# Kernel tuning notes

Measured on AMD Instinct MI355X. Metric: run time of the kernel, lower is better.

## Reference

```python
import jax, jax.numpy as jnp
import numpy as np
import math

HEIGHT = 256
THRESH = int(HEIGHT / (2 * math.sqrt(2)))  # 90, as in Spectral_Discriminator.__init__
EPS = 1e-8


def _radial_bins(h, w):
    # Static (numpy) integer radius of each pixel from the spectrum center.
    y, x = np.indices((h, w))
    cx, cy = (w - 1) / 2.0, (h - 1) / 2.0
    r = np.hypot(x - cx, y - cy)
    r_int = r.astype(np.int64).ravel()           # [h*w]
    nbins = int(r_int.max()) + 1                 # ~ h/sqrt(2) + 1 bins
    return jnp.asarray(r_int), nbins


def get_fft_feature(x):
    # x: [B, 3, H, W] -> azimuthally averaged log power spectrum [B, nbins]
    gray = 0.2989 * x[:, 0] + 0.5870 * x[:, 1] + 0.1140 * x[:, 2]   # [B,H,W]
    f = jnp.fft.fft2(gray)                                           # complex64
    mag = jnp.log(jnp.abs(f) + EPS)                                  # log magnitude
    mag = jnp.fft.fftshift(mag, axes=(-2, -1))                       # center DC
    B, h, w = mag.shape
    r_int, nbins = _radial_bins(h, w)
    flat = mag.reshape(B, -1)                                        # [B, h*w]
    # radial (azimuthal-average) binning: segment mean by integer radius
    sums = jax.vmap(lambda v: jax.ops.segment_sum(v, r_int, num_segments=nbins))(flat)
    counts = jax.ops.segment_sum(jnp.ones((h * w,), jnp.float32), r_int, num_segments=nbins)
    prof = sums / counts                                             # [B, nbins]
    # per-sample min-max normalization (NaN if max==min; masked by caller)
    mn = prof.min(axis=1, keepdims=True)
    mx = prof.max(axis=1, keepdims=True)
    return (prof - mn) / (mx - mn)


def setup_inputs() -> dict:
    key = jax.random.key(0)
    k1, k2 = jax.random.split(key)
    x = jax.random.normal(k1, (128, 3, HEIGHT, HEIGHT), dtype=jnp.float32)
    w = jax.random.normal(k2, (1, THRESH), dtype=jnp.float32) * (1.0 / math.sqrt(THRESH))
    b = jnp.zeros((1,), dtype=jnp.float32)
    return {"x": x, "w": w, "b": b}


def reference(x, w, b):
    feat = get_fft_feature(x)                          # [B, nbins]
    feat = jnp.where(jnp.isnan(feat), 0.0, feat)       # nan-masking as in forward
    feat = feat[:, -THRESH:]                           # high-frequency tail
    return feat @ w.T + b                              # [B, 1]
```

## Files before the change

kernel.cpp:

```cpp
#include <hip/hip_runtime.h>
#include <hip/hip_fp16.h>
#include <math.h>

#define NB 128
#define N 256
#define NBINS 181
#define THRESH 90
#define RS 136
#define GS 264
#define BST 137

__device__ __forceinline__ int br4(int i) {
    return ((i&1)<<3) | ((i&2)<<1) | ((i&4)>>1) | ((i&8)>>3);
}

__device__ const float TW16R[8] = { 1.f,  0.92387953f,  0.70710678f,  0.38268343f,
                                    0.f, -0.38268343f, -0.70710678f, -0.92387953f };
__device__ const float TW16I[8] = { 0.f, -0.38268343f, -0.70710678f, -0.92387953f,
                                   -1.f, -0.92387953f, -0.70710678f, -0.38268343f };
__device__ const float W256R[16] = {
    1.00000000f, 0.99969882f, 0.99879546f, 0.99729046f, 0.99518473f, 0.99247953f,
    0.98917651f, 0.98527764f, 0.98078528f, 0.97570213f, 0.97003125f, 0.96377607f,
    0.95694034f, 0.94952818f, 0.94154407f, 0.93299280f };
__device__ const float W256I[16] = {
    -0.00000000f, -0.02454123f, -0.04906767f, -0.07356456f, -0.09801714f, -0.12241068f,
    -0.14673047f, -0.17096189f, -0.19509032f, -0.21910124f, -0.24298018f, -0.26671276f,
    -0.29028468f, -0.31368174f, -0.33688985f, -0.35989504f };

__device__ __forceinline__ void fft16(float2 v[16]) {
    #pragma unroll
    for (int s = 0; s < 4; ++s) {
        const int half = 1 << s;
        #pragma unroll
        for (int gg = 0; gg < 16; gg += 2*half) {
            #pragma unroll
            for (int j = 0; j < half; ++j) {
                const float wr = TW16R[j << (3 - s)];
                const float wi = TW16I[j << (3 - s)];
                float2 a = v[gg + j], b = v[gg + j + half];
                float tr = b.x*wr - b.y*wi;
                float ti = b.x*wi + b.y*wr;
                v[gg + j]        = make_float2(a.x + tr, a.y + ti);
                v[gg + j + half] = make_float2(a.x - tr, a.y - ti);
            }
        }
    }
}

__device__ __forceinline__ void twiddle256(float2 v[16], int l) {
    const float c = W256R[l], s = W256I[l];
    float wr = c, wi = s;
    #pragma unroll
    for (int k = 1; k < 16; ++k) {
        float xr = v[k].x, xi = v[k].y;
        v[k] = make_float2(xr*wr - xi*wi, xr*wi + xi*wr);
        float nr = wr*c - wi*s;
        float ni = wr*s + wi*c;
        wr = nr; wi = ni;
    }
}

__global__ __launch_bounds__(128) void row_fft_kernel(const float* __restrict__ x,
                                                      __half2* __restrict__ F) {
    __shared__ float2 zbuf[8*GS];

    const int t = threadIdx.x;
    const int b = blockIdx.y;
    const int pbase = blockIdx.x * 8;

    const int cidx = t & 63;
    const int sub  = t >> 6;
    const float* xb = x + (size_t)b * 3 * N * N;
    #pragma unroll
    for (int i = 0; i < 4; ++i) {
        int p  = i*2 + sub;
        int r0 = (pbase + p) * 2;
        const float* p0 = xb + (size_t)r0 * N + cidx*4;
        float4 a0 = *(const float4*)(p0);
        float4 a1 = *(const float4*)(p0 + N*N);
        float4 a2 = *(const float4*)(p0 + 2*N*N);
        float4 b0 = *(const float4*)(p0 + N);
        float4 b1 = *(const float4*)(p0 + N*N + N);
        float4 b2 = *(const float4*)(p0 + 2*N*N + N);
        float gx[4], gy[4];
        #pragma unroll
        for (int j = 0; j < 4; ++j) {
            gx[j] = 0.2989f*((&a0.x)[j]) + 0.587f*((&a1.x)[j]) + 0.114f*((&a2.x)[j]);
            gy[j] = 0.2989f*((&b0.x)[j]) + 0.587f*((&b1.x)[j]) + 0.114f*((&b2.x)[j]);
        }
        *(float4*)&zbuf[p*GS + cidx*4]     = make_float4(gx[0], gy[0], gx[1], gy[1]);
        *(float4*)&zbuf[p*GS + cidx*4 + 2] = make_float4(gx[2], gy[2], gx[3], gy[3]);
    }
    __syncthreads();

    const int g = t >> 4, l = t & 15;
    float2 v[16];
    #pragma unroll
    for (int i = 0; i < 16; ++i) v[i] = zbuf[g*GS + 16*br4(i) + l];
    fft16(v);
    twiddle256(v, l);
    #pragma unroll
    for (int k = 0; k < 16; ++k) zbuf[g*GS + k*16 + ((l + k) & 15)] = v[k];
    #pragma unroll
    for (int i = 0; i < 16; ++i) v[i] = zbuf[g*GS + l*16 + ((br4(i) + l) & 15)];
    fft16(v);

    const int lane = t & 63;
    const int src  = (lane & 48) | ((16 - l) & 15);
    __half2* o0 = F + ((size_t)b * N + (size_t)(pbase + g) * 2) * RS;
    __half2* o1 = o0 + RS;
    #pragma unroll
    for (int k2 = 0; k2 < 8; ++k2) {
        float2 zm_s;
        zm_s.x = __shfl(v[15 - k2].x, src, 64);
        zm_s.y = __shfl(v[15 - k2].y, src, 64);
        float2 zm = (l == 0) ? v[(16 - k2) & 15] : zm_s;
        float2 z  = v[k2];
        int k = l + 16*k2;
        o0[k] = __floats2half2_rn(0.5f*(z.x + zm.x), 0.5f*(z.y - zm.y));
        o1[k] = __floats2half2_rn(0.5f*(z.y + zm.y), 0.5f*(zm.x - z.x));
    }
    if (l == 0) {
        float2 z = v[8];
        o0[128] = __floats2half2_rn(z.x, 0.f);
        o1[128] = __floats2half2_rn(z.y, 0.f);
    }
}

__global__ __launch_bounds__(256) void col_fft_kernel(const __half2* __restrict__ F,
                                                      __half* __restrict__ mag) {
    __shared__ float2 sbuf[16*272];
    __shared__ __half mag_lds[16*256];

    const int t = threadIdx.x;
    const int b  = blockIdx.y;
    const int cg = blockIdx.x;

    {
        const int c = t & 15, q = t >> 4;
        const int colr = cg*16 + c;
        const bool vread = (colr <= 128);
        const __half2* base = F + (size_t)b * N * RS;
        #pragma unroll
        for (int i = 0; i < 16; ++i) {
            int row = i*16 + q;
            float2 vv = vread ? __half22float2(base[(size_t)row * RS + colr])
                              : make_float2(0.f, 0.f);
            sbuf[row*17 + c] = vv;
        }
    }
    __syncthreads();

    const int g = t >> 4, l = t & 15;
    const int col = cg*16 + g;
    const bool valid = (col <= 128);
    float2 v[16];
    if (valid) {
        #pragma unroll
        for (int i = 0; i < 16; ++i) v[i] = sbuf[(16*br4(i) + l)*17 + g];
        fft16(v);
        twiddle256(v, l);
    }
    __syncthreads();

    if (valid) {
        #pragma unroll
        for (int k = 0; k < 16; ++k) sbuf[g*272 + k*17 + l] = v[k];
        #pragma unroll
        for (int i = 0; i < 16; ++i) v[i] = sbuf[g*272 + l*17 + br4(i)];
        fft16(v);
        #pragma unroll
        for (int k2 = 0; k2 < 16; ++k2) {
            float re = v[k2].x, im = v[k2].y;
            float mg = 0.5f * __logf(re*re + im*im + 1e-16f);
            int u = l + 16*k2;
            int idx = (u <= 127) ? (2*u + 1) : (2*(255 - u));
            mag_lds[g*256 + idx] = __float2half(mg);
        }
    }
    __syncthreads();

    #pragma unroll
    for (int j = 0; j < 2; ++j) {
        int flat = t + 256*j;
        int cl = flat >> 5, ch = flat & 31;
        if (cg < 8 || cl == 0) {
            int xs = (cg*16 + cl + 128) & 255;
            float4 d = *(const float4*)&mag_lds[cl*256 + ch*8];
            *(float4*)&mag[((size_t)b * 256 + xs) * 256 + ch*8] = d;
        }
    }
}

__global__ __launch_bounds__(512) void bin_kernel(const __half* __restrict__ mag,
                                                  float* __restrict__ prof) {
    __shared__ __half2 ml[129*BST];
    const int t = threadIdx.x;
    const int q = blockIdx.x;
    const int b = blockIdx.y;
    const int lane = t & 63, wv = t >> 6;

    {
        const __half2* mb2 = (const __half2*)(mag + (size_t)b * 65536);
        for (int flat = t; flat < 16512; flat += 512) {
            int ci = flat >> 7, ch = flat & 127;
            int xs = (ci == 0) ? 0 : 127 + ci;
            ml[ci*BST + ch] = mb2[(size_t)xs*128 + ch];
        }
    }
    __syncthreads();

    for (int r = q + 4*wv; r < NBINS; r += 32) {
        float sum = 0.0f; int cn = 0;
        const float rr0 = (float)(r*r);
        const float rr1 = (float)((r+1)*(r+1));
        #pragma unroll
        for (int xi = 0; xi < 4; ++xi) {
            int xs = lane + 64*xi;
            float dx = (float)xs - 127.5f;
            float dx2 = dx*dx;
            float hi2 = rr1 - dx2;
            if (hi2 <= 0.0f) continue;
            float lo2 = rr0 - dx2;
            int mlo = 0;
            if (lo2 > 0.0f) mlo = (int)ceilf(sqrtf(lo2) - 0.5f);
            int mhi = (int)ceilf(sqrtf(hi2) - 0.5f);
            if (mhi > 128) mhi = 128;
            if (mlo >= mhi) continue;
            cn += 2*(mhi - mlo);
            const bool mirror = (xs >= 1) && (xs <= 127);
            int ci, jlo, jhi, aHi, bLo;
            if (!mirror) {
                ci = (xs == 0) ? 0 : xs - 127;
                jlo = mlo; jhi = mhi; aHi = mhi; bLo = mlo;
            } else {
                ci = 129 - xs;
                jlo = ((mlo > 0) ? mlo : 1) - 1;
                jhi = ((mhi < 128) ? mhi : 127) + 1;
                aHi = mhi - 1; bLo = mlo + 1;
            }
            const __half2* fp = &ml[ci*BST];
            if (mirror) {
                if (mlo == 0)   sum += __half2float(__high2half(fp[0]));
                if (mhi == 128) sum += __half2float(__low2half(fp[127]));
            }
            float s0=0.f, s1=0.f, s2=0.f, s3=0.f;
            int j = jlo;
            for (; j + 4 <= jhi; j += 4) {
                float2 a  = __half22float2(fp[j]);
                float2 bb = __half22float2(fp[j+1]);
                float2 c  = __half22float2(fp[j+2]);
                float2 d  = __half22float2(fp[j+3]);
                s0 += ((j   < aHi) ? a.x  : 0.f) + ((j   >= bLo) ? a.y  : 0.f);
                s1 += ((j+1 < aHi) ? bb.x : 0.f) + ((j+1 >= bLo) ? bb.y : 0.f);
                s2 += ((j+2 < aHi) ? c.x  : 0.f) + ((j+2 >= bLo) ? c.y  : 0.f);
                s3 += ((j+3 < aHi) ? d.x  : 0.f) + ((j+3 >= bLo) ? d.y  : 0.f);
            }
            for (; j < jhi; ++j) {
                float2 a = __half22float2(fp[j]);
                s0 += ((j < aHi) ? a.x : 0.f) + ((j >= bLo) ? a.y : 0.f);
            }
            sum += (s0 + s1) + (s2 + s3);
        }
        #pragma unroll
        for (int msk = 32; msk >= 1; msk >>= 1) {
            sum += __shfl_xor(sum, msk);
            cn  += __shfl_xor(cn,  msk);
        }
        if (lane == 0) prof[b*NBINS + r] = sum / (float)cn;
    }
}

__global__ __launch_bounds__(256) void final_kernel(const float* __restrict__ prof,
                                                    const float* __restrict__ w,
                                                    const float* __restrict__ bias,
                                                    float* __restrict__ out) {
    __shared__ float red[16];
    const int t = threadIdx.x, b = blockIdx.x;
    const int lane = t & 63, wv = t >> 6;

    float vv = (t < NBINS) ? prof[b*NBINS + t] : prof[b*NBINS];
    float mn = vv, mx = vv;
    #pragma unroll
    for (int m = 32; m >= 1; m >>= 1) {
        mn = fminf(mn, __shfl_xor(mn, m));
        mx = fmaxf(mx, __shfl_xor(mx, m));
    }
    if (lane == 0) { red[wv] = mn; red[4 + wv] = mx; }
    __syncthreads();
    if (t == 0) {
        red[8] = fminf(fminf(red[0], red[1]), fminf(red[2], red[3]));
        red[9] = fmaxf(fmaxf(red[4], red[5]), fmaxf(red[6], red[7]));
    }
    __syncthreads();
    const float mnv = red[8], mxv = red[9];

    float part = 0.0f;
    if (t < THRESH) {
        float f = (prof[b*NBINS + (NBINS - THRESH) + t] - mnv) / (mxv - mnv);
        if (f != f) f = 0.0f;
        part = f * w[t];
    }
    #pragma unroll
    for (int m = 32; m >= 1; m >>= 1) part += __shfl_xor(part, m);
    if (lane == 0) red[10 + wv] = part;
    __syncthreads();
    if (t == 0) out[b] = red[10] + red[11] + red[12] + red[13] + bias[0];
}

extern "C" void kernel_launch(void* const* d_in, const int* in_sizes, int n_in,
                              void* d_out, int out_size, void* d_ws, size_t ws_size,
                              hipStream_t stream) {
    const float* x    = (const float*)d_in[0];
    const float* w    = (const float*)d_in[1];
    const float* bias = (const float*)d_in[2];
    float* out = (float*)d_out;

    char* ws = (char*)d_ws;
    __half2* F  = (__half2*)ws;
    __half* mag = (__half*)(ws + (size_t)NB * N * RS * sizeof(__half2));
    float* prof = (float*)(ws + (size_t)NB * N * RS * sizeof(__half2)
                              + (size_t)NB * 256 * 256 * sizeof(__half));

    row_fft_kernel<<<dim3(16, NB), 128, 0, stream>>>(x, F);
    col_fft_kernel<<<dim3(9, NB), 256, 0, stream>>>(F, mag);
    bin_kernel<<<dim3(4, NB), 512, 0, stream>>>(mag, prof);
    final_kernel<<<NB, 256, 0, stream>>>(prof, w, bias, out);
}
```

Measured before the change: 72.12 us.

## Fuse column FFT with radial binning using atomics, drop magnitude buffer

After: 84.36 us. 17.0% more time.

```diff
diff --git a/kernel.cpp b/kernel.cpp
--- a/kernel.cpp
+++ b/kernel.cpp
@@ -8,7 +8,7 @@
 #define THRESH 90
 #define RS 136
 #define GS 264
-#define BST 137
+#define MCS 260
 
 __device__ __forceinline__ int br4(int i) {
     return ((i&1)<<3) | ((i&2)<<1) | ((i&4)>>1) | ((i&8)>>3);
@@ -127,10 +127,10 @@
     }
 }
 
-__global__ __launch_bounds__(256) void col_fft_kernel(const __half2* __restrict__ F,
-                                                      __half* __restrict__ mag) {
-    __shared__ float2 sbuf[16*272];
-    __shared__ __half mag_lds[16*256];
+__global__ __launch_bounds__(256) void colbin_kernel(const __half2* __restrict__ F,
+                                                     float* __restrict__ prof) {
+    __shared__ __half2 sbuf[16*272];
+    __shared__ __half mag_lds[16*MCS];
 
     const int t = threadIdx.x;
     const int b  = blockIdx.y;
@@ -144,9 +144,8 @@
         #pragma unroll
         for (int i = 0; i < 16; ++i) {
             int row = i*16 + q;
-            float2 vv = vread ? __half22float2(base[(size_t)row * RS + colr])
-                              : make_float2(0.f, 0.f);
-            sbuf[row*17 + c] = vv;
+            sbuf[row*17 + c] = vread ? base[(size_t)row * RS + colr]
+                                     : __floats2half2_rn(0.f, 0.f);
         }
     }
     __syncthreads();
@@ -157,7 +156,7 @@
     float2 v[16];
     if (valid) {
         #pragma unroll
-        for (int i = 0; i < 16; ++i) v[i] = sbuf[(16*br4(i) + l)*17 + g];
+        for (int i = 0; i < 16; ++i) v[i] = __half22float2(sbuf[(16*br4(i) + l)*17 + g]);
         fft16(v);
         twiddle256(v, l);
     }
@@ -165,9 +164,9 @@
 
     if (valid) {
         #pragma unroll
-        for (int k = 0; k < 16; ++k) sbuf[g*272 + k*17 + l] = v[k];
-        #pragma unroll
-        for (int i = 0; i < 16; ++i) v[i] = sbuf[g*272 + l*17 + br4(i)];
+        for (int k = 0; k < 16; ++k) sbuf[g*272 + k*17 + l] = __float22half2_rn(v[k]);
+        #pragma unroll
+        for (int i = 0; i < 16; ++i) v[i] = __half22float2(sbuf[g*272 + l*17 + br4(i)]);
         fft16(v);
         #pragma unroll
         for (int k2 = 0; k2 < 16; ++k2) {
@@ -175,111 +174,101 @@
             float mg = 0.5f * __logf(re*re + im*im + 1e-16f);
             int u = l + 16*k2;
             int idx = (u <= 127) ? (2*u + 1) : (2*(255 - u));
-            mag_lds[g*256 + idx] = __float2half(mg);
-        }
-    }
-    __syncthreads();
-
-    #pragma unroll
-    for (int j = 0; j < 2; ++j) {
-        int flat = t + 256*j;
-        int cl = flat >> 5, ch = flat & 31;
-        if (cg < 8 || cl == 0) {
-            int xs = (cg*16 + cl + 128) & 255;
-            float4 d = *(const float4*)&mag_lds[cl*256 + ch*8];
-            *(float4*)&mag[((size_t)b * 256 + xs) * 256 + ch*8] = d;
-        }
-    }
-}
-
-__global__ __launch_bounds__(512) void bin_kernel(const __half* __restrict__ mag,
-                                                  float* __restrict__ prof) {
-    __shared__ __half2 ml[129*BST];
-    const int t = threadIdx.x;
-    const int q = blockIdx.x;
-    const int b = blockIdx.y;
+            mag_lds[g*MCS + idx] = __float2half(mg);
+        }
+    }
+    __syncthreads();
+
     const int lane = t & 63, wv = t >> 6;
-
-    {
-        const __half2* mb2 = (const __half2*)(mag + (size_t)b * 65536);
-        for (int flat = t; flat < 16512; flat += 512) {
-            int ci = flat >> 7, ch = flat & 127;
-            int xs = (ci == 0) ? 0 : 127 + ci;
-            ml[ci*BST + ch] = mb2[(size_t)xs*128 + ch];
-        }
-    }
-    __syncthreads();
-
-    for (int r = q + 4*wv; r < NBINS; r += 32) {
-        float sum = 0.0f; int cn = 0;
-        const float rr0 = (float)(r*r);
-        const float rr1 = (float)((r+1)*(r+1));
-        #pragma unroll
-        for (int xi = 0; xi < 4; ++xi) {
-            int xs = lane + 64*xi;
-            float dx = (float)xs - 127.5f;
-            float dx2 = dx*dx;
+    const int h = lane >> 5;
+    const int p = lane & 31;
+    const int c = p & 15;
+    const bool mir = (p >= 16);
+    const int ci = cg*16 + c;
+    const bool pvalid = mir ? (ci >= 1 && ci <= 127) : (ci <= 128);
+    const float adx = mir ? ((float)ci - 0.5f)
+                          : ((ci == 128) ? 127.5f : ((float)ci + 0.5f));
+    const float dx2 = adx * adx;
+    const __half2* fp = (const __half2*)&mag_lds[c*MCS];
+
+    for (int r = wv*2 + h; r < NBINS; r += 8) {
+        float sum = 0.0f;
+        if (pvalid) {
+            const float rr0 = (float)(r*r);
+            const float rr1 = (float)((r+1)*(r+1));
             float hi2 = rr1 - dx2;
+            if (hi2 > 0.0f) {
+                float lo2 = rr0 - dx2;
+                int mlo = 0;
+                if (lo2 > 0.0f) mlo = (int)ceilf(sqrtf(lo2) - 0.5f);
+                int mhi = (int)ceilf(sqrtf(hi2) - 0.5f);
+                if (mhi > 128) mhi = 128;
+                if (mlo < mhi) {
+                    int jlo, jhi, aHi, bLo;
+                    if (!mir) { jlo = mlo; jhi = mhi; aHi = mhi; bLo = mlo; }
+                    else {
+                        jlo = ((mlo > 0) ? mlo : 1) - 1;
+                        jhi = ((mhi < 128) ? mhi : 127) + 1;
+                        aHi = mhi - 1; bLo = mlo + 1;
+                        if (mlo == 0)   sum += __half2float(__high2half(fp[0]));
+                        if (mhi == 128) sum += __half2float(__low2half(fp[127]));
+                    }
+                    float s0=0.f, s1=0.f, s2=0.f, s3=0.f;
+                    int j = jlo;
+                    for (; j + 4 <= jhi; j += 4) {
+                        float2 a  = __half22float2(fp[j]);
+                        float2 bb = __half22float2(fp[j+1]);
+                        float2 cc = __half22float2(fp[j+2]);
+                        float2 d  = __half22float2(fp[j+3]);
+                        s0 += ((j   < aHi) ? a.x  : 0.f) + ((j   >= bLo) ? a.y  : 0.f);
+                        s1 += ((j+1 < aHi) ? bb.x : 0.f) + ((j+1 >= bLo) ? bb.y : 0.f);
+                        s2 += ((j+2 < aHi) ? cc.x : 0.f) + ((j+2 >= bLo) ? cc.y : 0.f);
+                        s3 += ((j+3 < aHi) ? d.x  : 0.f) + ((j+3 >= bLo) ? d.y  : 0.f);
+                    }
+                    for (; j < jhi; ++j) {
+                        float2 a = __half22float2(fp[j]);
+                        s0 += ((j < aHi) ? a.x : 0.f) + ((j >= bLo) ? a.y : 0.f);
+                    }
+                    sum += (s0 + s1) + (s2 + s3);
+                }
+            }
+        }
+        #pragma unroll
+        for (int msk = 16; msk >= 1; msk >>= 1) sum += __shfl_xor(sum, msk);
+        if (p == 0) atomicAdd(&prof[b*NBINS + r], sum);
+    }
+}
+
+__global__ __launch_bounds__(256) void final_kernel(const float* __restrict__ prof,
+                                                    const float* __restrict__ w,
+                                                    const float* __restrict__ bias,
+                                                    float* __restrict__ out) {
+    __shared__ float pr[192];
+    __shared__ float red[16];
+    const int t = threadIdx.x, b = blockIdx.x;
+    const int lane = t & 63, wv = t >> 6;
+
+    if (t < NBINS) {
+        const float rr0 = (float)(t*t);
+        const float rr1 = (float)((t+1)*(t+1));
+        int cnt = 0;
+        for (int a = 0; a < 128; ++a) {
+            float adx = (float)a + 0.5f;
+            float d2 = adx*adx;
+            float hi2 = rr1 - d2;
             if (hi2 <= 0.0f) continue;
-            float lo2 = rr0 - dx2;
+            float lo2 = rr0 - d2;
             int mlo = 0;
             if (lo2 > 0.0f) mlo = (int)ceilf(sqrtf(lo2) - 0.5f);
             int mhi = (int)ceilf(sqrtf(hi2) - 0.5f);
             if (mhi > 128) mhi = 128;
-            if (mlo >= mhi) continue;
-            cn += 2*(mhi - mlo);
-            const bool mirror = (xs >= 1) && (xs <= 127);
-            int ci, jlo, jhi, aHi, bLo;
-            if (!mirror) {
-                ci = (xs == 0) ? 0 : xs - 127;
-                jlo = mlo; jhi = mhi; aHi = mhi; bLo = mlo;
-            } else {
-                ci = 129 - xs;
-                jlo = ((mlo > 0) ? mlo : 1) - 1;
-                jhi = ((mhi < 128) ? mhi : 127) + 1;
-                aHi = mhi - 1; bLo = mlo + 1;
-            }
-            const __half2* fp = &ml[ci*BST];
-            if (mirror) {
-                if (mlo == 0)   sum += __half2float(__high2half(fp[0]));
-                if (mhi == 128) sum += __half2float(__low2half(fp[127]));
-            }
-            float s0=0.f, s1=0.f, s2=0.f, s3=0.f;
-            int j = jlo;
-            for (; j + 4 <= jhi; j += 4) {
-                float2 a  = __half22float2(fp[j]);
-                float2 bb = __half22float2(fp[j+1]);
-                float2 c  = __half22float2(fp[j+2]);
-                float2 d  = __half22float2(fp[j+3]);
-                s0 += ((j   < aHi) ? a.x  : 0.f) + ((j   >= bLo) ? a.y  : 0.f);
-                s1 += ((j+1 < aHi) ? bb.x : 0.f) + ((j+1 >= bLo) ? bb.y : 0.f);
-                s2 += ((j+2 < aHi) ? c.x  : 0.f) + ((j+2 >= bLo) ? c.y  : 0.f);
-                s3 += ((j+3 < aHi) ? d.x  : 0.f) + ((j+3 >= bLo) ? d.y  : 0.f);
-            }
-            for (; j < jhi; ++j) {
-                float2 a = __half22float2(fp[j]);
-                s0 += ((j < aHi) ? a.x : 0.f) + ((j >= bLo) ? a.y : 0.f);
-            }
-            sum += (s0 + s1) + (s2 + s3);
-        }
-        #pragma unroll
-        for (int msk = 32; msk >= 1; msk >>= 1) {
-            sum += __shfl_xor(sum, msk);
-            cn  += __shfl_xor(cn,  msk);
-        }
-        if (lane == 0) prof[b*NBINS + r] = sum / (float)cn;
-    }
-}
-
-__global__ __launch_bounds__(256) void final_kernel(const float* __restrict__ prof,
-                                                    const float* __restrict__ w,
-                                                    const float* __restrict__ bias,
-                                                    float* __restrict__ out) {
-    __shared__ float red[16];
-    const int t = threadIdx.x, b = blockIdx.x;
-    const int lane = t & 63, wv = t >> 6;
-
-    float vv = (t < NBINS) ? prof[b*NBINS + t] : prof[b*NBINS];
+            if (mlo < mhi) cnt += (mhi - mlo);
+        }
+        pr[t] = prof[b*NBINS + t] / (float)(4*cnt);
+    }
+    __syncthreads();
+
+    float vv = (t < NBINS) ? pr[t] : pr[0];
     float mn = vv, mx = vv;
     #pragma unroll
     for (int m = 32; m >= 1; m >>= 1) {
@@ -297,7 +286,7 @@
 
     float part = 0.0f;
     if (t < THRESH) {
-        float f = (prof[b*NBINS + (NBINS - THRESH) + t] - mnv) / (mxv - mnv);
+        float f = (pr[(NBINS - THRESH) + t] - mnv) / (mxv - mnv);
         if (f != f) f = 0.0f;
         part = f * w[t];
     }
@@ -317,13 +306,11 @@
     float* out = (float*)d_out;
 
     char* ws = (char*)d_ws;
-    __half2* F  = (__half2*)ws;
-    __half* mag = (__half*)(ws + (size_t)NB * N * RS * sizeof(__half2));
-    float* prof = (float*)(ws + (size_t)NB * N * RS * sizeof(__half2)
-                              + (size_t)NB * 256 * 256 * sizeof(__half));
-
+    __half2* F = (__half2*)ws;
+    float* prof = (float*)(ws + (size_t)NB * N * RS * sizeof(__half2));
+
+    hipMemsetAsync(prof, 0, (size_t)NB * NBINS * sizeof(float), stream);
     row_fft_kernel<<<dim3(16, NB), 128, 0, stream>>>(x, F);
-    col_fft_kernel<<<dim3(9, NB), 256, 0, stream>>>(F, mag);
-    bin_kernel<<<dim3(4, NB), 512, 0, stream>>>(mag, prof);
+    colbin_kernel<<<dim3(9, NB), 256, 0, stream>>>(F, prof);
     final_kernel<<<NB, 256, 0, stream>>>(prof, w, bias, out);
 }
```
